# Performance work log

Hardware: AMD Instinct MI355X
Metric: run time of the kernel (lower is better)

Reference implementation:

```python
import jax, jax.numpy as jnp
import numpy as np

B, N, D, FUSE, A = 512, 1024, 1024, 1024, 256


def setup_inputs() -> dict:
    key = jax.random.key(0)
    ks = jax.random.split(key, 6)
    return {
        "confounder_set": jax.random.normal(ks[0], (N, D), dtype=jnp.float32),
        "fuse_rep": jax.random.normal(ks[1], (B, FUSE), dtype=jnp.float32),
        "probabilities": jax.random.uniform(ks[2], (1, N), dtype=jnp.float32),
        "Wq": jax.random.normal(ks[3], (FUSE, A), dtype=jnp.float32) / np.sqrt(FUSE),
        "Wk": jax.random.normal(ks[4], (D, A), dtype=jnp.float32) / np.sqrt(D),
        "wt": jax.random.normal(ks[5], (A,), dtype=jnp.float32) / np.sqrt(A),
    }


def reference(confounder_set, fuse_rep, probabilities, Wq, Wk, wt):
    # query: [B, A], key: [N, A]
    q = fuse_rep @ Wq
    k = confounder_set @ Wk
    # broadcasted add + tanh -> [B, N, A]
    fuse = jnp.tanh(q[:, None, :] + k[None, :, :])
    # scoring linear -> [B, N]
    scores = jnp.einsum("bna,a->bn", fuse, wt)
    attn = jax.nn.softmax(scores, axis=1)           # [B, N]
    probs = probabilities[0]                        # [N]  (transpose(0,1) of [1,N])
    # probability-weighted confounder sum -> [B, D]
    fin = jnp.einsum("bn,nd->bd", attn * probs[None, :], confounder_set)
    return fin
```

## Files before the change

kernel.cpp:

```cpp
#include <hip/hip_runtime.h>
#include <hip/hip_bf16.h>

#define B 512
#define N 1024
#define D 1024
#define FUSE 1024
#define A 256

typedef float f32x4 __attribute__((ext_vector_type(4)));
typedef short bf16x8 __attribute__((ext_vector_type(8)));
typedef unsigned short u16x4 __attribute__((ext_vector_type(4)));

__device__ __forceinline__ float fast_exp2(float x) { return __builtin_amdgcn_exp2f(x); }
__device__ __forceinline__ float fast_rcp(float x)  { return __builtin_amdgcn_rcpf(x); }

static constexpr float TANH_C = 2.8853900817779268f;
static constexpr float LOG2E  = 1.4426950408889634f;

__device__ __forceinline__ unsigned short f2bf(float x) {
    __hip_bfloat16 h = __float2bfloat16(x);
    return *reinterpret_cast<unsigned short*>(&h);
}

__global__ __launch_bounds__(256) void cast_kernel(
    const float* __restrict__ fuse, const float* __restrict__ conf,
    const float* __restrict__ Wq, const float* __restrict__ Wk,
    short* __restrict__ fuse_bf, short* __restrict__ conf_bf,
    short* __restrict__ confT, short* __restrict__ WqT, short* __restrict__ WkT)
{
    __shared__ float tile[64 * 65];
    int bid = blockIdx.x;
    const float* src; short* dstS = nullptr; short* dstT = nullptr;
    int r0, c0, spitch; float scale = 1.0f;
    if (bid < 128) {
        src = fuse; dstS = fuse_bf; spitch = FUSE;
        r0 = (bid >> 4) * 64; c0 = (bid & 15) * 64;
    } else if (bid < 384) {
        int b = bid - 128; src = conf; dstS = conf_bf; dstT = confT; spitch = D;
        r0 = (b >> 4) * 64; c0 = (b & 15) * 64;
    } else if (bid < 448) {
        int b = bid - 384; src = Wq; dstT = WqT; spitch = A; scale = TANH_C;
        r0 = (b >> 2) * 64; c0 = (b & 3) * 64;
    } else {
        int b = bid - 448; src = Wk; dstT = WkT; spitch = A; scale = TANH_C;
        r0 = (b >> 2) * 64; c0 = (b & 3) * 64;
    }
    const int tr = threadIdx.x >> 4, tc = (threadIdx.x & 15) * 4;

    f32x4 v[4];
#pragma unroll
    for (int i = 0; i < 4; ++i) {
        v[i] = *(const f32x4*)(src + (size_t)(r0 + tr + 16 * i) * spitch + c0 + tc);
#pragma unroll
        for (int j = 0; j < 4; ++j) v[i][j] *= scale;
    }
    if (dstS) {
#pragma unroll
        for (int i = 0; i < 4; ++i) {
            u16x4 o;
#pragma unroll
            for (int j = 0; j < 4; ++j) o[j] = f2bf(v[i][j]);
            *(u16x4*)(dstS + (size_t)(r0 + tr + 16 * i) * spitch + c0 + tc) = o;
        }
    }
    if (dstT) {
#pragma unroll
        for (int i = 0; i < 4; ++i)
#pragma unroll
            for (int j = 0; j < 4; ++j) tile[(tr + 16 * i) * 65 + tc + j] = v[i][j];
        __syncthreads();
#pragma unroll
        for (int i = 0; i < 4; ++i) {
            int orow = tr + 16 * i;
            u16x4 o;
#pragma unroll
            for (int j = 0; j < 4; ++j) o[j] = f2bf(tile[(tc + j) * 65 + orow]);
            *(u16x4*)(dstT + (size_t)(c0 + orow) * 1024 + r0 + tc) = o;
        }
    }
}

__device__ __forceinline__ void gemm64_pipe(
    const short* __restrict__ Ag, const short* __restrict__ Btg,
    float* __restrict__ C, int K, int ldc, int m0, int n0,
    char* As, char* Bs)
{
    const int tid = threadIdx.x;
    const int w = tid >> 6, l = tid & 63;
    const int wm = w >> 1, wn = w & 1;
    const int lr = l & 15;
    const int cr = (l >> 4) * 4;
    const int rsub = l >> 3;
    const int ssrc = ((l & 7) ^ rsub) << 3;

    auto stage = [&](int buf, int k0) {
#pragma unroll
        for (int p = 0; p < 2; ++p) {
            int chunk = (w << 1) | p;
            int row = (chunk << 3) | rsub;
            int ldsoff = (buf << 13) | (chunk << 10);
            __builtin_amdgcn_global_load_lds(
                (const __attribute__((address_space(1))) unsigned int*)
                    (Ag + (size_t)(m0 + row) * K + k0 + ssrc),
                (__attribute__((address_space(3))) unsigned int*)(As + ldsoff),
                16, 0, 0);
            __builtin_amdgcn_global_load_lds(
                (const __attribute__((address_space(1))) unsigned int*)
                    (Btg + (size_t)(n0 + row) * K + k0 + ssrc),
                (__attribute__((address_space(3))) unsigned int*)(Bs + ldsoff),
                16, 0, 0);
        }
    };

    f32x4 acc[2][2] = {};
    const int nt = K >> 6;

    stage(0, 0);
    asm volatile("s_waitcnt vmcnt(0)" ::: "memory");
    __builtin_amdgcn_s_barrier();

    int cur = 0;
    for (int t = 0; t < nt; ++t) {
        if (t + 1 < nt) stage(cur ^ 1, (t + 1) << 6);

        const char* Ab = As + (cur << 13);
        const char* Bb = Bs + (cur << 13);
        bf16x8 af[2][2], bq[2][2];
#pragma unroll
        for (int ks = 0; ks < 2; ++ks)
#pragma unroll
            for (int i = 0; i < 2; ++i) {
                int j = ks * 64 + ((l >> 4) << 4);
                int r = wm * 32 + i * 16 + lr;
                af[i][ks] = *(const bf16x8*)(Ab + r * 128 + (j ^ ((r & 7) << 4)));
                int c = wn * 32 + i * 16 + lr;
                bq[i][ks] = *(const bf16x8*)(Bb + c * 128 + (j ^ ((c & 7) << 4)));
            }
#pragma unroll
        for (int ks = 0; ks < 2; ++ks)
#pragma unroll
            for (int am = 0; am < 2; ++am)
#pragma unroll
                for (int bn = 0; bn < 2; ++bn)
                    acc[am][bn] = __builtin_amdgcn_mfma_f32_16x16x32_bf16(
                        af[am][ks], bq[bn][ks], acc[am][bn], 0, 0, 0);

        asm volatile("s_waitcnt vmcnt(0)" ::: "memory");
        __builtin_amdgcn_s_barrier();
        cur ^= 1;
    }

#pragma unroll
    for (int am = 0; am < 2; ++am)
#pragma unroll
        for (int bn = 0; bn < 2; ++bn) {
            float* cp = C + (size_t)(m0 + wm * 32 + am * 16 + cr) * ldc
                          + n0 + wn * 32 + bn * 16 + lr;
#pragma unroll
            for (int r = 0; r < 4; ++r) cp[(size_t)r * ldc] = acc[am][bn][r];
        }
}

__global__ __launch_bounds__(256) void qk_gemm_kernel(
    const short* __restrict__ fuse_bf, const short* __restrict__ conf_bf,
    const short* __restrict__ WqT, const short* __restrict__ WkT,
    float* __restrict__ qbuf, float* __restrict__ kbuf)
{
    __shared__ char As[16384];
    __shared__ char Bs[16384];
    int bid = blockIdx.x;
    if (bid < 32) {
        gemm64_pipe(fuse_bf, WqT, qbuf, FUSE, A, (bid >> 2) * 64, (bid & 3) * 64, As, Bs);
    } else {
        bid -= 32;
        gemm64_pipe(conf_bf, WkT, kbuf, D, A, (bid >> 2) * 64, (bid & 3) * 64, As, Bs);
    }
}

__global__ __launch_bounds__(256) void fin_gemm_kernel(
    const short* __restrict__ wb, const short* __restrict__ confT,
    float* __restrict__ out)
{
    __shared__ char As[16384];
    __shared__ char Bs[16384];
    gemm64_pipe(wb, confT, out, N, D, blockIdx.y * 64, blockIdx.x * 64, As, Bs);
}

__global__ __launch_bounds__(256) void scores_kernel(
    const float* __restrict__ qbuf, const float* __restrict__ kbuf,
    const float* __restrict__ wt, float* __restrict__ s)
{
    __shared__ f32x4 qs[32 * 64];
    __shared__ f32x4 ks[32 * 64];
    const int tid = threadIdx.x;
    const int b0 = blockIdx.x * 32;
    const int n0 = blockIdx.y * 32;

    const f32x4* q4 = (const f32x4*)qbuf + (size_t)b0 * 64;
    const f32x4* k4 = (const f32x4*)kbuf + (size_t)n0 * 64;
#pragma unroll
    for (int j = 0; j < 8; ++j) {
        int idx = tid + j * 256;
        int r = idx >> 6, c = idx & 63;
        qs[idx] = q4[idx];
        ks[r * 64 + (c ^ (r & 15))] = k4[idx];
    }
    __syncthreads();

    const int bl = tid >> 5;
    const int nl = tid & 31;
    const f32x4* wt4 = (const f32x4*)wt;

    float acc0 = 0.f, acc1 = 0.f, acc2 = 0.f, acc3 = 0.f;
    for (int a4 = 0; a4 < 64; ++a4) {
        f32x4 kv = ks[nl * 64 + (a4 ^ (nl & 15))];
        f32x4 wv = wt4[a4];
        f32x4 q0 = qs[(bl) * 64 + a4];
        f32x4 q1 = qs[(bl + 8) * 64 + a4];
        f32x4 q2 = qs[(bl + 16) * 64 + a4];
        f32x4 q3 = qs[(bl + 24) * 64 + a4];
#pragma unroll
        for (int c = 0; c < 4; ++c) {
            float kc = kv[c], wc = wv[c];
            acc0 += wc * fast_rcp(fast_exp2(q0[c] + kc) + 1.0f);
            acc1 += wc * fast_rcp(fast_exp2(q1[c] + kc) + 1.0f);
            acc2 += wc * fast_rcp(fast_exp2(q2[c] + kc) + 1.0f);
            acc3 += wc * fast_rcp(fast_exp2(q3[c] + kc) + 1.0f);
        }
    }
    s[(size_t)(b0 + bl) * N + n0 + nl]      = -2.0f * acc0;
    s[(size_t)(b0 + bl + 8) * N + n0 + nl]  = -2.0f * acc1;
    s[(size_t)(b0 + bl + 16) * N + n0 + nl] = -2.0f * acc2;
    s[(size_t)(b0 + bl + 24) * N + n0 + nl] = -2.0f * acc3;
}

__global__ __launch_bounds__(256) void softmax_kernel(
    const float* __restrict__ s, const float* __restrict__ probs,
    short* __restrict__ wbuf)
{
    const int b = blockIdx.x, tid = threadIdx.x;
    const f32x4* s4 = (const f32x4*)(s + (size_t)b * N);
    f32x4 v = s4[tid];

    float m = fmaxf(fmaxf(v[0], v[1]), fmaxf(v[2], v[3]));
    for (int off = 32; off > 0; off >>= 1) m = fmaxf(m, __shfl_xor(m, off));
    __shared__ float redm[4];
    __shared__ float reds[4];
    const int wid = tid >> 6, lane = tid & 63;
    if (lane == 0) redm[wid] = m;
    __syncthreads();
    m = fmaxf(fmaxf(redm[0], redm[1]), fmaxf(redm[2], redm[3]));

    f32x4 e;
#pragma unroll
    for (int c = 0; c < 4; ++c) e[c] = fast_exp2((v[c] - m) * LOG2E);
    float sum = e[0] + e[1] + e[2] + e[3];
    for (int off = 32; off > 0; off >>= 1) sum += __shfl_xor(sum, off);
    if (lane == 0) reds[wid] = sum;
    __syncthreads();
    sum = reds[0] + reds[1] + reds[2] + reds[3];

    const float inv = fast_rcp(sum);
    const f32x4* p4 = (const f32x4*)probs;
    f32x4 p = p4[tid];
    u16x4 o;
#pragma unroll
    for (int c = 0; c < 4; ++c) o[c] = f2bf(e[c] * inv * p[c]);
    ((u16x4*)(wbuf + (size_t)b * N))[tid] = o;
}

extern "C" void kernel_launch(void* const* d_in, const int* in_sizes, int n_in,
                              void* d_out, int out_size, void* d_ws, size_t ws_size,
                              hipStream_t stream) {
    const float* conf     = (const float*)d_in[0];
    const float* fuse_rep = (const float*)d_in[1];
    const float* probs    = (const float*)d_in[2];
    const float* Wq       = (const float*)d_in[3];
    const float* Wk       = (const float*)d_in[4];
    const float* wt       = (const float*)d_in[5];
    float* out = (float*)d_out;

    char* w = (char*)d_ws;
    float* qbuf   = (float*)(w);
    float* kbuf   = (float*)(w + 524288);
    float* sbuf   = (float*)(w + 1572864);
    short* fuse_bf= (short*)(w + 3670016);
    short* conf_bf= (short*)(w + 4718592);
    short* confT  = (short*)(w + 6815744);
    short* WqT    = (short*)(w + 8912896);
    short* WkT    = (short*)(w + 9437184);
    short* wbuf   = (short*)(w);

    hipLaunchKernelGGL(cast_kernel, dim3(512), dim3(256), 0, stream,
                       fuse_rep, conf, Wq, Wk, fuse_bf, conf_bf, confT, WqT, WkT);
    hipLaunchKernelGGL(qk_gemm_kernel, dim3(96), dim3(256), 0, stream,
                       fuse_bf, conf_bf, WqT, WkT, qbuf, kbuf);
    hipLaunchKernelGGL(scores_kernel, dim3(B / 32, N / 32), dim3(256), 0, stream,
                       qbuf, kbuf, wt, sbuf);
    hipLaunchKernelGGL(softmax_kernel, dim3(B), dim3(256), 0, stream,
                       sbuf, probs, wbuf);
    hipLaunchKernelGGL(fin_gemm_kernel, dim3(D / 64, B / 64), dim3(256), 0, stream,
                       wbuf, confT, out);
}
```

Before: 129.5 us.

## Fuse all stages into a persistent kernel with grid barriers and split-K QK GEMM

```diff
diff --git a/kernel.cpp b/kernel.cpp
--- a/kernel.cpp
+++ b/kernel.cpp
@@ -22,67 +22,29 @@
     return *reinterpret_cast<unsigned short*>(&h);
 }
 
-__global__ __launch_bounds__(256) void cast_kernel(
-    const float* __restrict__ fuse, const float* __restrict__ conf,
-    const float* __restrict__ Wq, const float* __restrict__ Wk,
-    short* __restrict__ fuse_bf, short* __restrict__ conf_bf,
-    short* __restrict__ confT, short* __restrict__ WqT, short* __restrict__ WkT)
-{
-    __shared__ float tile[64 * 65];
-    int bid = blockIdx.x;
-    const float* src; short* dstS = nullptr; short* dstT = nullptr;
-    int r0, c0, spitch; float scale = 1.0f;
-    if (bid < 128) {
-        src = fuse; dstS = fuse_bf; spitch = FUSE;
-        r0 = (bid >> 4) * 64; c0 = (bid & 15) * 64;
-    } else if (bid < 384) {
-        int b = bid - 128; src = conf; dstS = conf_bf; dstT = confT; spitch = D;
-        r0 = (b >> 4) * 64; c0 = (b & 15) * 64;
-    } else if (bid < 448) {
-        int b = bid - 384; src = Wq; dstT = WqT; spitch = A; scale = TANH_C;
-        r0 = (b >> 2) * 64; c0 = (b & 3) * 64;
-    } else {
-        int b = bid - 448; src = Wk; dstT = WkT; spitch = A; scale = TANH_C;
-        r0 = (b >> 2) * 64; c0 = (b & 3) * 64;
-    }
-    const int tr = threadIdx.x >> 4, tc = (threadIdx.x & 15) * 4;
-
-    f32x4 v[4];
-#pragma unroll
-    for (int i = 0; i < 4; ++i) {
-        v[i] = *(const f32x4*)(src + (size_t)(r0 + tr + 16 * i) * spitch + c0 + tc);
-#pragma unroll
-        for (int j = 0; j < 4; ++j) v[i][j] *= scale;
-    }
-    if (dstS) {
-#pragma unroll
-        for (int i = 0; i < 4; ++i) {
-            u16x4 o;
-#pragma unroll
-            for (int j = 0; j < 4; ++j) o[j] = f2bf(v[i][j]);
-            *(u16x4*)(dstS + (size_t)(r0 + tr + 16 * i) * spitch + c0 + tc) = o;
-        }
-    }
-    if (dstT) {
-#pragma unroll
-        for (int i = 0; i < 4; ++i)
-#pragma unroll
-            for (int j = 0; j < 4; ++j) tile[(tr + 16 * i) * 65 + tc + j] = v[i][j];
-        __syncthreads();
-#pragma unroll
-        for (int i = 0; i < 4; ++i) {
-            int orow = tr + 16 * i;
-            u16x4 o;
-#pragma unroll
-            for (int j = 0; j < 4; ++j) o[j] = f2bf(tile[(tc + j) * 65 + orow]);
-            *(u16x4*)(dstT + (size_t)(c0 + orow) * 1024 + r0 + tc) = o;
-        }
-    }
+struct SMemGemm  { char As[16384]; char Bs[16384]; };
+struct SMemSc    { f32x4 qs[32 * 32]; f32x4 ks[32 * 32]; };
+union SMem {
+    float castTile[64 * 65];
+    SMemGemm g;
+    SMemSc   sc;
+    float red[8];
+};
+
+__device__ __forceinline__ void grid_barrier(unsigned* bar, unsigned target) {
+    __syncthreads();
+    __threadfence();
+    if (threadIdx.x == 0) {
+        atomicAdd(bar, 1u);
+        while (atomicAdd(bar, 0u) < target) __builtin_amdgcn_s_sleep(4);
+    }
+    __syncthreads();
+    __threadfence();
 }
 
 __device__ __forceinline__ void gemm64_pipe(
     const short* __restrict__ Ag, const short* __restrict__ Btg,
-    float* __restrict__ C, int K, int ldc, int m0, int n0,
+    float* __restrict__ C, int lda, int Klen, int ldc, int m0, int n0,
     char* As, char* Bs)
 {
     const int tid = threadIdx.x;
@@ -101,19 +63,19 @@
             int ldsoff = (buf << 13) | (chunk << 10);
             __builtin_amdgcn_global_load_lds(
                 (const __attribute__((address_space(1))) unsigned int*)
-                    (Ag + (size_t)(m0 + row) * K + k0 + ssrc),
+                    (Ag + (size_t)(m0 + row) * lda + k0 + ssrc),
                 (__attribute__((address_space(3))) unsigned int*)(As + ldsoff),
                 16, 0, 0);
             __builtin_amdgcn_global_load_lds(
                 (const __attribute__((address_space(1))) unsigned int*)
-                    (Btg + (size_t)(n0 + row) * K + k0 + ssrc),
+                    (Btg + (size_t)(n0 + row) * lda + k0 + ssrc),
                 (__attribute__((address_space(3))) unsigned int*)(Bs + ldsoff),
                 16, 0, 0);
         }
     };
 
     f32x4 acc[2][2] = {};
-    const int nt = K >> 6;
+    const int nt = Klen >> 6;
 
     stage(0, 0);
     asm volatile("s_waitcnt vmcnt(0)" ::: "memory");
@@ -161,112 +123,176 @@
         }
 }
 
-__global__ __launch_bounds__(256) void qk_gemm_kernel(
-    const short* __restrict__ fuse_bf, const short* __restrict__ conf_bf,
-    const short* __restrict__ WqT, const short* __restrict__ WkT,
-    float* __restrict__ qbuf, float* __restrict__ kbuf)
+__global__ __launch_bounds__(256, 2) void mega_kernel(
+    const float* __restrict__ conf, const float* __restrict__ fuse,
+    const float* __restrict__ probs,
+    const float* __restrict__ Wq, const float* __restrict__ Wk,
+    const float* __restrict__ wt,
+    float* __restrict__ out,
+    short* __restrict__ fuse_bf, short* __restrict__ conf_bf,
+    short* __restrict__ confT, short* __restrict__ WqT, short* __restrict__ WkT,
+    float* __restrict__ qpart, float* __restrict__ kpart,
+    float* __restrict__ sbuf, short* __restrict__ wbuf,
+    unsigned* __restrict__ bar)
 {
-    __shared__ char As[16384];
-    __shared__ char Bs[16384];
-    int bid = blockIdx.x;
-    if (bid < 32) {
-        gemm64_pipe(fuse_bf, WqT, qbuf, FUSE, A, (bid >> 2) * 64, (bid & 3) * 64, As, Bs);
-    } else {
-        bid -= 32;
-        gemm64_pipe(conf_bf, WkT, kbuf, D, A, (bid >> 2) * 64, (bid & 3) * 64, As, Bs);
-    }
-}
-
-__global__ __launch_bounds__(256) void fin_gemm_kernel(
-    const short* __restrict__ wb, const short* __restrict__ confT,
-    float* __restrict__ out)
-{
-    __shared__ char As[16384];
-    __shared__ char Bs[16384];
-    gemm64_pipe(wb, confT, out, N, D, blockIdx.y * 64, blockIdx.x * 64, As, Bs);
-}
-
-__global__ __launch_bounds__(256) void scores_kernel(
-    const float* __restrict__ qbuf, const float* __restrict__ kbuf,
-    const float* __restrict__ wt, float* __restrict__ s)
-{
-    __shared__ f32x4 qs[32 * 64];
-    __shared__ f32x4 ks[32 * 64];
+    __shared__ SMem smem;
+    const int bid = blockIdx.x;
     const int tid = threadIdx.x;
-    const int b0 = blockIdx.x * 32;
-    const int n0 = blockIdx.y * 32;
-
-    const f32x4* q4 = (const f32x4*)qbuf + (size_t)b0 * 64;
-    const f32x4* k4 = (const f32x4*)kbuf + (size_t)n0 * 64;
-#pragma unroll
-    for (int j = 0; j < 8; ++j) {
-        int idx = tid + j * 256;
-        int r = idx >> 6, c = idx & 63;
-        qs[idx] = q4[idx];
-        ks[r * 64 + (c ^ (r & 15))] = k4[idx];
-    }
-    __syncthreads();
-
-    const int bl = tid >> 5;
-    const int nl = tid & 31;
-    const f32x4* wt4 = (const f32x4*)wt;
-
-    float acc0 = 0.f, acc1 = 0.f, acc2 = 0.f, acc3 = 0.f;
-    for (int a4 = 0; a4 < 64; ++a4) {
-        f32x4 kv = ks[nl * 64 + (a4 ^ (nl & 15))];
-        f32x4 wv = wt4[a4];
-        f32x4 q0 = qs[(bl) * 64 + a4];
-        f32x4 q1 = qs[(bl + 8) * 64 + a4];
-        f32x4 q2 = qs[(bl + 16) * 64 + a4];
-        f32x4 q3 = qs[(bl + 24) * 64 + a4];
-#pragma unroll
-        for (int c = 0; c < 4; ++c) {
-            float kc = kv[c], wc = wv[c];
-            acc0 += wc * fast_rcp(fast_exp2(q0[c] + kc) + 1.0f);
-            acc1 += wc * fast_rcp(fast_exp2(q1[c] + kc) + 1.0f);
-            acc2 += wc * fast_rcp(fast_exp2(q2[c] + kc) + 1.0f);
-            acc3 += wc * fast_rcp(fast_exp2(q3[c] + kc) + 1.0f);
-        }
-    }
-    s[(size_t)(b0 + bl) * N + n0 + nl]      = -2.0f * acc0;
-    s[(size_t)(b0 + bl + 8) * N + n0 + nl]  = -2.0f * acc1;
-    s[(size_t)(b0 + bl + 16) * N + n0 + nl] = -2.0f * acc2;
-    s[(size_t)(b0 + bl + 24) * N + n0 + nl] = -2.0f * acc3;
-}
-
-__global__ __launch_bounds__(256) void softmax_kernel(
-    const float* __restrict__ s, const float* __restrict__ probs,
-    short* __restrict__ wbuf)
-{
-    const int b = blockIdx.x, tid = threadIdx.x;
-    const f32x4* s4 = (const f32x4*)(s + (size_t)b * N);
-    f32x4 v = s4[tid];
-
-    float m = fmaxf(fmaxf(v[0], v[1]), fmaxf(v[2], v[3]));
-    for (int off = 32; off > 0; off >>= 1) m = fmaxf(m, __shfl_xor(m, off));
-    __shared__ float redm[4];
-    __shared__ float reds[4];
-    const int wid = tid >> 6, lane = tid & 63;
-    if (lane == 0) redm[wid] = m;
-    __syncthreads();
-    m = fmaxf(fmaxf(redm[0], redm[1]), fmaxf(redm[2], redm[3]));
-
-    f32x4 e;
-#pragma unroll
-    for (int c = 0; c < 4; ++c) e[c] = fast_exp2((v[c] - m) * LOG2E);
-    float sum = e[0] + e[1] + e[2] + e[3];
-    for (int off = 32; off > 0; off >>= 1) sum += __shfl_xor(sum, off);
-    if (lane == 0) reds[wid] = sum;
-    __syncthreads();
-    sum = reds[0] + reds[1] + reds[2] + reds[3];
-
-    const float inv = fast_rcp(sum);
-    const f32x4* p4 = (const f32x4*)probs;
-    f32x4 p = p4[tid];
-    u16x4 o;
-#pragma unroll
-    for (int c = 0; c < 4; ++c) o[c] = f2bf(e[c] * inv * p[c]);
-    ((u16x4*)(wbuf + (size_t)b * N))[tid] = o;
+
+    {
+        const float* src; short* dstS = nullptr; short* dstT = nullptr;
+        int r0, c0, spitch; float scale = 1.0f;
+        if (bid < 128) {
+            src = fuse; dstS = fuse_bf; spitch = FUSE;
+            r0 = (bid >> 4) * 64; c0 = (bid & 15) * 64;
+        } else if (bid < 384) {
+            int b = bid - 128; src = conf; dstS = conf_bf; dstT = confT; spitch = D;
+            r0 = (b >> 4) * 64; c0 = (b & 15) * 64;
+        } else if (bid < 448) {
+            int b = bid - 384; src = Wq; dstT = WqT; spitch = A; scale = TANH_C;
+            r0 = (b >> 2) * 64; c0 = (b & 3) * 64;
+        } else {
+            int b = bid - 448; src = Wk; dstT = WkT; spitch = A; scale = TANH_C;
+            r0 = (b >> 2) * 64; c0 = (b & 3) * 64;
+        }
+        const int tr = tid >> 4, tc = (tid & 15) * 4;
+        f32x4 v[4];
+#pragma unroll
+        for (int i = 0; i < 4; ++i) {
+            v[i] = *(const f32x4*)(src + (size_t)(r0 + tr + 16 * i) * spitch + c0 + tc);
+#pragma unroll
+            for (int j = 0; j < 4; ++j) v[i][j] *= scale;
+        }
+        if (dstS) {
+#pragma unroll
+            for (int i = 0; i < 4; ++i) {
+                u16x4 o;
+#pragma unroll
+                for (int j = 0; j < 4; ++j) o[j] = f2bf(v[i][j]);
+                *(u16x4*)(dstS + (size_t)(r0 + tr + 16 * i) * spitch + c0 + tc) = o;
+            }
+        }
+        if (dstT) {
+#pragma unroll
+            for (int i = 0; i < 4; ++i)
+#pragma unroll
+                for (int j = 0; j < 4; ++j)
+                    smem.castTile[(tr + 16 * i) * 65 + tc + j] = v[i][j];
+            __syncthreads();
+#pragma unroll
+            for (int i = 0; i < 4; ++i) {
+                int orow = tr + 16 * i;
+                u16x4 o;
+#pragma unroll
+                for (int j = 0; j < 4; ++j) o[j] = f2bf(smem.castTile[(tc + j) * 65 + orow]);
+                *(u16x4*)(dstT + (size_t)(c0 + orow) * 1024 + r0 + tc) = o;
+            }
+        }
+    }
+    grid_barrier(bar, 512);
+
+    if (bid < 192) {
+        int khalf = (bid >= 96) ? 1 : 0;
+        int tile = bid - khalf * 96;
+        const short* Aop; const short* Bop; float* Cp; int m0, n0;
+        if (tile < 32) {
+            Aop = fuse_bf; Bop = WqT; Cp = qpart + (size_t)khalf * B * A;
+            m0 = (tile >> 2) * 64; n0 = (tile & 3) * 64;
+        } else {
+            int t2 = tile - 32;
+            Aop = conf_bf; Bop = WkT; Cp = kpart + (size_t)khalf * N * A;
+            m0 = (t2 >> 2) * 64; n0 = (t2 & 3) * 64;
+        }
+        gemm64_pipe(Aop + khalf * 512, Bop + khalf * 512, Cp,
+                    1024, 512, A, m0, n0, smem.g.As, smem.g.Bs);
+    }
+    grid_barrier(bar, 1024);
+
+    {
+        const int b0 = (bid & 15) * 32;
+        const int n0 = (bid >> 4) * 32;
+        const f32x4* qp0 = (const f32x4*)qpart;
+        const f32x4* qp1 = qp0 + (size_t)B * A / 4;
+        const f32x4* kp0 = (const f32x4*)kpart;
+        const f32x4* kp1 = kp0 + (size_t)N * A / 4;
+        const f32x4* wt4 = (const f32x4*)wt;
+        const int bl = tid >> 5;
+        const int nl = tid & 31;
+
+        float acc0 = 0.f, acc1 = 0.f, acc2 = 0.f, acc3 = 0.f;
+#pragma unroll
+        for (int c = 0; c < 2; ++c) {
+#pragma unroll
+            for (int j = 0; j < 4; ++j) {
+                int idx = tid + j * 256;
+                int r = idx >> 5, col = idx & 31;
+                size_t qsrc = (size_t)(b0 + r) * 64 + c * 32 + col;
+                size_t ksrc = (size_t)(n0 + r) * 64 + c * 32 + col;
+                smem.sc.qs[r * 32 + col] = qp0[qsrc] + qp1[qsrc];
+                smem.sc.ks[r * 32 + (col ^ (r & 15))] = kp0[ksrc] + kp1[ksrc];
+            }
+            __syncthreads();
+            for (int a4 = 0; a4 < 32; ++a4) {
+                f32x4 kv = smem.sc.ks[nl * 32 + (a4 ^ (nl & 15))];
+                f32x4 wv = wt4[c * 32 + a4];
+                f32x4 q0 = smem.sc.qs[(bl) * 32 + a4];
+                f32x4 q1 = smem.sc.qs[(bl + 8) * 32 + a4];
+                f32x4 q2 = smem.sc.qs[(bl + 16) * 32 + a4];
+                f32x4 q3 = smem.sc.qs[(bl + 24) * 32 + a4];
+#pragma unroll
+                for (int cc = 0; cc < 4; ++cc) {
+                    float kc = kv[cc], wc = wv[cc];
+                    acc0 += wc * fast_rcp(fast_exp2(q0[cc] + kc) + 1.0f);
+                    acc1 += wc * fast_rcp(fast_exp2(q1[cc] + kc) + 1.0f);
+                    acc2 += wc * fast_rcp(fast_exp2(q2[cc] + kc) + 1.0f);
+                    acc3 += wc * fast_rcp(fast_exp2(q3[cc] + kc) + 1.0f);
+                }
+            }
+            __syncthreads();
+        }
+        sbuf[(size_t)(b0 + bl) * N + n0 + nl]      = -2.0f * acc0;
+        sbuf[(size_t)(b0 + bl + 8) * N + n0 + nl]  = -2.0f * acc1;
+        sbuf[(size_t)(b0 + bl + 16) * N + n0 + nl] = -2.0f * acc2;
+        sbuf[(size_t)(b0 + bl + 24) * N + n0 + nl] = -2.0f * acc3;
+    }
+    grid_barrier(bar, 1536);
+
+    {
+        const int b = bid;
+        const f32x4* s4 = (const f32x4*)(sbuf + (size_t)b * N);
+        f32x4 v = s4[tid];
+        float m = fmaxf(fmaxf(v[0], v[1]), fmaxf(v[2], v[3]));
+        for (int off = 32; off > 0; off >>= 1) m = fmaxf(m, __shfl_xor(m, off));
+        const int wid = tid >> 6, lane = tid & 63;
+        if (lane == 0) smem.red[wid] = m;
+        __syncthreads();
+        m = fmaxf(fmaxf(smem.red[0], smem.red[1]), fmaxf(smem.red[2], smem.red[3]));
+
+        f32x4 e;
+#pragma unroll
+        for (int c = 0; c < 4; ++c) e[c] = fast_exp2((v[c] - m) * LOG2E);
+        float sum = e[0] + e[1] + e[2] + e[3];
+        for (int off = 32; off > 0; off >>= 1) sum += __shfl_xor(sum, off);
+        __syncthreads();
+        if (lane == 0) smem.red[4 + wid] = sum;
+        __syncthreads();
+        sum = smem.red[4] + smem.red[5] + smem.red[6] + smem.red[7];
+
+        const float inv = fast_rcp(sum);
+        const f32x4* p4 = (const f32x4*)probs;
+        f32x4 p = p4[tid];
+        u16x4 o;
+#pragma unroll
+        for (int c = 0; c < 4; ++c) o[c] = f2bf(e[c] * inv * p[c]);
+        ((u16x4*)(wbuf + (size_t)b * N))[tid] = o;
+    }
+    grid_barrier(bar, 2048);
+
+    if (bid < 128) {
+        int x = bid & 15, y = bid >> 4;
+        gemm64_pipe(wbuf, confT, out, 1024, 1024, D, y * 64, x * 64,
+                    smem.g.As, smem.g.Bs);
+    }
 }
 
 extern "C" void kernel_launch(void* const* d_in, const int* in_sizes, int n_in,
@@ -281,24 +307,20 @@
     float* out = (float*)d_out;
 
     char* w = (char*)d_ws;
-    float* qbuf   = (float*)(w);
-    float* kbuf   = (float*)(w + 524288);
-    float* sbuf   = (float*)(w + 1572864);
-    short* fuse_bf= (short*)(w + 3670016);
-    short* conf_bf= (short*)(w + 4718592);
-    short* confT  = (short*)(w + 6815744);
-    short* WqT    = (short*)(w + 8912896);
-    short* WkT    = (short*)(w + 9437184);
-    short* wbuf   = (short*)(w);
-
-    hipLaunchKernelGGL(cast_kernel, dim3(512), dim3(256), 0, stream,
-                       fuse_rep, conf, Wq, Wk, fuse_bf, conf_bf, confT, WqT, WkT);
-    hipLaunchKernelGGL(qk_gemm_kernel, dim3(96), dim3(256), 0, stream,
-                       fuse_bf, conf_bf, WqT, WkT, qbuf, kbuf);
-    hipLaunchKernelGGL(scores_kernel, dim3(B / 32, N / 32), dim3(256), 0, stream,
-                       qbuf, kbuf, wt, sbuf);
-    hipLaunchKernelGGL(softmax_kernel, dim3(B), dim3(256), 0, stream,
-                       sbuf, probs, wbuf);
-    hipLaunchKernelGGL(fin_gemm_kernel, dim3(D / 64, B / 64), dim3(256), 0, stream,
-                       wbuf, confT, out);
-}
+    float* qpart  = (float*)(w);
+    float* kpart  = (float*)(w + (1u << 20));
+    float* sbuf   = (float*)(w + (3u << 20));
+    short* fuse_bf= (short*)(w + (5u << 20));
+    short* conf_bf= (short*)(w + (6u << 20));
+    short* confT  = (short*)(w + (8u << 20));
+    short* WqT    = (short*)(w + (10u << 20));
+    short* WkT    = (short*)(w + (10u << 20) + (512u << 10));
+    short* wbuf   = (short*)(w + (11u << 20));
+    unsigned* bar = (unsigned*)(w + (12u << 20));
+
+    hipMemsetAsync(bar, 0, sizeof(unsigned), stream);
+    hipLaunchKernelGGL(mega_kernel, dim3(512), dim3(256), 0, stream,
+                       conf, fuse_rep, probs, Wq, Wk, wt, out,
+                       fuse_bf, conf_bf, confT, WqT, WkT,
+                       qpart, kpart, sbuf, wbuf, bar);
+}
```

New measurement: 505.2 us. 290% more time.

## Retile GEMMs to 32x64, widen scores tile, drop softmax max pass

Applied to the files above, without the earlier changes.

```diff
diff --git a/kernel.cpp b/kernel.cpp
--- a/kernel.cpp
+++ b/kernel.cpp
@@ -80,9 +80,9 @@
     }
 }
 
-__device__ __forceinline__ void gemm64_pipe(
+__device__ __forceinline__ void gemm32x64_pipe(
     const short* __restrict__ Ag, const short* __restrict__ Btg,
-    float* __restrict__ C, int K, int ldc, int m0, int n0,
+    float* __restrict__ C, int ldc, int m0, int n0,
     char* As, char* Bs)
 {
     const int tid = threadIdx.x;
@@ -94,71 +94,60 @@
     const int ssrc = ((l & 7) ^ rsub) << 3;
 
     auto stage = [&](int buf, int k0) {
+        {
+            int row = (w << 3) | rsub;
+            __builtin_amdgcn_global_load_lds(
+                (const __attribute__((address_space(1))) unsigned int*)
+                    (Ag + (size_t)(m0 + row) * 1024 + k0 + ssrc),
+                (__attribute__((address_space(3))) unsigned int*)(As + (buf << 12) + (w << 10)),
+                16, 0, 0);
+        }
 #pragma unroll
         for (int p = 0; p < 2; ++p) {
             int chunk = (w << 1) | p;
             int row = (chunk << 3) | rsub;
-            int ldsoff = (buf << 13) | (chunk << 10);
             __builtin_amdgcn_global_load_lds(
                 (const __attribute__((address_space(1))) unsigned int*)
-                    (Ag + (size_t)(m0 + row) * K + k0 + ssrc),
-                (__attribute__((address_space(3))) unsigned int*)(As + ldsoff),
+                    (Btg + (size_t)(n0 + row) * 1024 + k0 + ssrc),
+                (__attribute__((address_space(3))) unsigned int*)(Bs + (buf << 13) + (chunk << 10)),
                 16, 0, 0);
-            __builtin_amdgcn_global_load_lds(
-                (const __attribute__((address_space(1))) unsigned int*)
-                    (Btg + (size_t)(n0 + row) * K + k0 + ssrc),
-                (__attribute__((address_space(3))) unsigned int*)(Bs + ldsoff),
-                16, 0, 0);
         }
     };
 
-    f32x4 acc[2][2] = {};
-    const int nt = K >> 6;
-
+    f32x4 acc[2] = {};
     stage(0, 0);
     asm volatile("s_waitcnt vmcnt(0)" ::: "memory");
     __builtin_amdgcn_s_barrier();
 
     int cur = 0;
-    for (int t = 0; t < nt; ++t) {
-        if (t + 1 < nt) stage(cur ^ 1, (t + 1) << 6);
-
-        const char* Ab = As + (cur << 13);
+    for (int t = 0; t < 16; ++t) {
+        if (t < 15) stage(cur ^ 1, (t + 1) << 6);
+
+        const char* Ab = As + (cur << 12);
         const char* Bb = Bs + (cur << 13);
-        bf16x8 af[2][2], bq[2][2];
-#pragma unroll
-        for (int ks = 0; ks < 2; ++ks)
+#pragma unroll
+        for (int ks = 0; ks < 2; ++ks) {
+            int j = ks * 64 + ((l >> 4) << 4);
+            int r = wm * 16 + lr;
+            bf16x8 af = *(const bf16x8*)(Ab + r * 128 + (j ^ ((r & 7) << 4)));
 #pragma unroll
             for (int i = 0; i < 2; ++i) {
-                int j = ks * 64 + ((l >> 4) << 4);
-                int r = wm * 32 + i * 16 + lr;
-                af[i][ks] = *(const bf16x8*)(Ab + r * 128 + (j ^ ((r & 7) << 4)));
                 int c = wn * 32 + i * 16 + lr;
-                bq[i][ks] = *(const bf16x8*)(Bb + c * 128 + (j ^ ((c & 7) << 4)));
+                bf16x8 bq = *(const bf16x8*)(Bb + c * 128 + (j ^ ((c & 7) << 4)));
+                acc[i] = __builtin_amdgcn_mfma_f32_16x16x32_bf16(af, bq, acc[i], 0, 0, 0);
             }
-#pragma unroll
-        for (int ks = 0; ks < 2; ++ks)
-#pragma unroll
-            for (int am = 0; am < 2; ++am)
-#pragma unroll
-                for (int bn = 0; bn < 2; ++bn)
-                    acc[am][bn] = __builtin_amdgcn_mfma_f32_16x16x32_bf16(
-                        af[am][ks], bq[bn][ks], acc[am][bn], 0, 0, 0);
-
+        }
         asm volatile("s_waitcnt vmcnt(0)" ::: "memory");
         __builtin_amdgcn_s_barrier();
         cur ^= 1;
     }
 
 #pragma unroll
-    for (int am = 0; am < 2; ++am)
-#pragma unroll
-        for (int bn = 0; bn < 2; ++bn) {
-            float* cp = C + (size_t)(m0 + wm * 32 + am * 16 + cr) * ldc
-                          + n0 + wn * 32 + bn * 16 + lr;
-#pragma unroll
-            for (int r = 0; r < 4; ++r) cp[(size_t)r * ldc] = acc[am][bn][r];
-        }
+    for (int i = 0; i < 2; ++i) {
+        float* cp = C + (size_t)(m0 + wm * 16 + cr) * ldc + n0 + wn * 32 + i * 16 + lr;
+#pragma unroll
+        for (int r = 0; r < 4; ++r) cp[(size_t)r * ldc] = acc[i][r];
+    }
 }
 
 __global__ __launch_bounds__(256) void qk_gemm_kernel(
@@ -166,14 +155,14 @@
     const short* __restrict__ WqT, const short* __restrict__ WkT,
     float* __restrict__ qbuf, float* __restrict__ kbuf)
 {
-    __shared__ char As[16384];
+    __shared__ char As[8192];
     __shared__ char Bs[16384];
     int bid = blockIdx.x;
-    if (bid < 32) {
-        gemm64_pipe(fuse_bf, WqT, qbuf, FUSE, A, (bid >> 2) * 64, (bid & 3) * 64, As, Bs);
+    if (bid < 64) {
+        gemm32x64_pipe(fuse_bf, WqT, qbuf, A, (bid >> 2) * 32, (bid & 3) * 64, As, Bs);
     } else {
-        bid -= 32;
-        gemm64_pipe(conf_bf, WkT, kbuf, D, A, (bid >> 2) * 64, (bid & 3) * 64, As, Bs);
+        bid -= 64;
+        gemm32x64_pipe(conf_bf, WkT, kbuf, A, (bid >> 2) * 32, (bid & 3) * 64, As, Bs);
     }
 }
 
@@ -181,57 +170,77 @@
     const short* __restrict__ wb, const short* __restrict__ confT,
     float* __restrict__ out)
 {
-    __shared__ char As[16384];
+    __shared__ char As[8192];
     __shared__ char Bs[16384];
-    gemm64_pipe(wb, confT, out, N, D, blockIdx.y * 64, blockIdx.x * 64, As, Bs);
+    gemm32x64_pipe(wb, confT, out, D, blockIdx.y * 32, blockIdx.x * 64, As, Bs);
 }
 
 __global__ __launch_bounds__(256) void scores_kernel(
     const float* __restrict__ qbuf, const float* __restrict__ kbuf,
-    const float* __restrict__ wt, float* __restrict__ s)
-{
-    __shared__ f32x4 qs[32 * 64];
-    __shared__ f32x4 ks[32 * 64];
+    const float* __restrict__ wt, float* __restrict__ sbuf)
+{
+    __shared__ f32x4 qs[32 * 32];
+    __shared__ f32x4 ks[64 * 32];
     const int tid = threadIdx.x;
-    const int b0 = blockIdx.x * 32;
-    const int n0 = blockIdx.y * 32;
-
-    const f32x4* q4 = (const f32x4*)qbuf + (size_t)b0 * 64;
-    const f32x4* k4 = (const f32x4*)kbuf + (size_t)n0 * 64;
-#pragma unroll
-    for (int j = 0; j < 8; ++j) {
-        int idx = tid + j * 256;
-        int r = idx >> 6, c = idx & 63;
-        qs[idx] = q4[idx];
-        ks[r * 64 + (c ^ (r & 15))] = k4[idx];
-    }
-    __syncthreads();
-
+    const int bid = blockIdx.x;
+    const int b0 = (bid & 15) * 32;
+    const int n0 = (bid >> 4) * 64;
+
+    const f32x4* q4 = (const f32x4*)qbuf;
+    const f32x4* k4 = (const f32x4*)kbuf;
+    const f32x4* wt4 = (const f32x4*)wt;
     const int bl = tid >> 5;
     const int nl = tid & 31;
-    const f32x4* wt4 = (const f32x4*)wt;
-
-    float acc0 = 0.f, acc1 = 0.f, acc2 = 0.f, acc3 = 0.f;
-    for (int a4 = 0; a4 < 64; ++a4) {
-        f32x4 kv = ks[nl * 64 + (a4 ^ (nl & 15))];
-        f32x4 wv = wt4[a4];
-        f32x4 q0 = qs[(bl) * 64 + a4];
-        f32x4 q1 = qs[(bl + 8) * 64 + a4];
-        f32x4 q2 = qs[(bl + 16) * 64 + a4];
-        f32x4 q3 = qs[(bl + 24) * 64 + a4];
-#pragma unroll
-        for (int c = 0; c < 4; ++c) {
-            float kc = kv[c], wc = wv[c];
-            acc0 += wc * fast_rcp(fast_exp2(q0[c] + kc) + 1.0f);
-            acc1 += wc * fast_rcp(fast_exp2(q1[c] + kc) + 1.0f);
-            acc2 += wc * fast_rcp(fast_exp2(q2[c] + kc) + 1.0f);
-            acc3 += wc * fast_rcp(fast_exp2(q3[c] + kc) + 1.0f);
-        }
-    }
-    s[(size_t)(b0 + bl) * N + n0 + nl]      = -2.0f * acc0;
-    s[(size_t)(b0 + bl + 8) * N + n0 + nl]  = -2.0f * acc1;
-    s[(size_t)(b0 + bl + 16) * N + n0 + nl] = -2.0f * acc2;
-    s[(size_t)(b0 + bl + 24) * N + n0 + nl] = -2.0f * acc3;
+
+    float a00 = 0.f, a10 = 0.f, a20 = 0.f, a30 = 0.f;
+    float a01 = 0.f, a11 = 0.f, a21 = 0.f, a31 = 0.f;
+#pragma unroll
+    for (int c = 0; c < 2; ++c) {
+#pragma unroll
+        for (int j = 0; j < 4; ++j) {
+            int idx = tid + j * 256;
+            int r = idx >> 5, col = idx & 31;
+            qs[r * 32 + col] = q4[(size_t)(b0 + r) * 64 + c * 32 + col];
+        }
+#pragma unroll
+        for (int j = 0; j < 8; ++j) {
+            int idx = tid + j * 256;
+            int r = idx >> 5, col = idx & 31;
+            ks[r * 32 + (col ^ (r & 15))] = k4[(size_t)(n0 + r) * 64 + c * 32 + col];
+        }
+        __syncthreads();
+        for (int a4 = 0; a4 < 32; ++a4) {
+            int kx = a4 ^ (nl & 15);
+            f32x4 kv0 = ks[nl * 32 + kx];
+            f32x4 kv1 = ks[(nl + 32) * 32 + kx];
+            f32x4 wv = wt4[c * 32 + a4];
+            f32x4 q0 = qs[(bl) * 32 + a4];
+            f32x4 q1 = qs[(bl + 8) * 32 + a4];
+            f32x4 q2 = qs[(bl + 16) * 32 + a4];
+            f32x4 q3 = qs[(bl + 24) * 32 + a4];
+#pragma unroll
+            for (int cc = 0; cc < 4; ++cc) {
+                float k0 = kv0[cc], k1 = kv1[cc], wc = wv[cc];
+                a00 += wc * fast_rcp(fast_exp2(q0[cc] + k0) + 1.0f);
+                a10 += wc * fast_rcp(fast_exp2(q1[cc] + k0) + 1.0f);
+                a20 += wc * fast_rcp(fast_exp2(q2[cc] + k0) + 1.0f);
+                a30 += wc * fast_rcp(fast_exp2(q3[cc] + k0) + 1.0f);
+                a01 += wc * fast_rcp(fast_exp2(q0[cc] + k1) + 1.0f);
+                a11 += wc * fast_rcp(fast_exp2(q1[cc] + k1) + 1.0f);
+                a21 += wc * fast_rcp(fast_exp2(q2[cc] + k1) + 1.0f);
+                a31 += wc * fast_rcp(fast_exp2(q3[cc] + k1) + 1.0f);
+            }
+        }
+        __syncthreads();
+    }
+    sbuf[(size_t)(b0 + bl) * N + n0 + nl]           = -2.0f * a00;
+    sbuf[(size_t)(b0 + bl + 8) * N + n0 + nl]       = -2.0f * a10;
+    sbuf[(size_t)(b0 + bl + 16) * N + n0 + nl]      = -2.0f * a20;
+    sbuf[(size_t)(b0 + bl + 24) * N + n0 + nl]      = -2.0f * a30;
+    sbuf[(size_t)(b0 + bl) * N + n0 + 32 + nl]      = -2.0f * a01;
+    sbuf[(size_t)(b0 + bl + 8) * N + n0 + 32 + nl]  = -2.0f * a11;
+    sbuf[(size_t)(b0 + bl + 16) * N + n0 + 32 + nl] = -2.0f * a21;
+    sbuf[(size_t)(b0 + bl + 24) * N + n0 + 32 + nl] = -2.0f * a31;
 }
 
 __global__ __launch_bounds__(256) void softmax_kernel(
@@ -242,20 +251,13 @@
     const f32x4* s4 = (const f32x4*)(s + (size_t)b * N);
     f32x4 v = s4[tid];
 
-    float m = fmaxf(fmaxf(v[0], v[1]), fmaxf(v[2], v[3]));
-    for (int off = 32; off > 0; off >>= 1) m = fmaxf(m, __shfl_xor(m, off));
-    __shared__ float redm[4];
+    f32x4 e;
+#pragma unroll
+    for (int c = 0; c < 4; ++c) e[c] = fast_exp2(v[c] * LOG2E);
+    float sum = e[0] + e[1] + e[2] + e[3];
+    for (int off = 32; off > 0; off >>= 1) sum += __shfl_xor(sum, off);
     __shared__ float reds[4];
     const int wid = tid >> 6, lane = tid & 63;
-    if (lane == 0) redm[wid] = m;
-    __syncthreads();
-    m = fmaxf(fmaxf(redm[0], redm[1]), fmaxf(redm[2], redm[3]));
-
-    f32x4 e;
-#pragma unroll
-    for (int c = 0; c < 4; ++c) e[c] = fast_exp2((v[c] - m) * LOG2E);
-    float sum = e[0] + e[1] + e[2] + e[3];
-    for (int off = 32; off > 0; off >>= 1) sum += __shfl_xor(sum, off);
     if (lane == 0) reds[wid] = sum;
     __syncthreads();
     sum = reds[0] + reds[1] + reds[2] + reds[3];
@@ -282,23 +284,23 @@
 
     char* w = (char*)d_ws;
     float* qbuf   = (float*)(w);
-    float* kbuf   = (float*)(w + 524288);
-    float* sbuf   = (float*)(w + 1572864);
-    short* fuse_bf= (short*)(w + 3670016);
-    short* conf_bf= (short*)(w + 4718592);
-    short* confT  = (short*)(w + 6815744);
-    short* WqT    = (short*)(w + 8912896);
-    short* WkT    = (short*)(w + 9437184);
+    float* kbuf   = (float*)(w + (1u << 20));
+    float* sbuf   = (float*)(w + (3u << 20));
+    short* fuse_bf= (short*)(w + (5u << 20));
+    short* conf_bf= (short*)(w + (6u << 20));
+    short* confT  = (short*)(w + (8u << 20));
+    short* WqT    = (short*)(w + (10u << 20));
+    short* WkT    = (short*)(w + (10u << 20) + (512u << 10));
     short* wbuf   = (short*)(w);
 
     hipLaunchKernelGGL(cast_kernel, dim3(512), dim3(256), 0, stream,
                        fuse_rep, conf, Wq, Wk, fuse_bf, conf_bf, confT, WqT, WkT);
-    hipLaunchKernelGGL(qk_gemm_kernel, dim3(96), dim3(256), 0, stream,
+    hipLaunchKernelGGL(qk_gemm_kernel, dim3(192), dim3(256), 0, stream,
                        fuse_bf, conf_bf, WqT, WkT, qbuf, kbuf);
-    hipLaunchKernelGGL(scores_kernel, dim3(B / 32, N / 32), dim3(256), 0, stream,
+    hipLaunchKernelGGL(scores_kernel, dim3(256), dim3(256), 0, stream,
                        qbuf, kbuf, wt, sbuf);
     hipLaunchKernelGGL(softmax_kernel, dim3(B), dim3(256), 0, stream,
                        sbuf, probs, wbuf);
-    hipLaunchKernelGGL(fin_gemm_kernel, dim3(D / 64, B / 64), dim3(256), 0, stream,
+    hipLaunchKernelGGL(fin_gemm_kernel, dim3(D / 64, B / 32), dim3(256), 0, stream,
                        wbuf, confT, out);
 }
```

Result: slower. 135.8 us (+4.8%).
